# Kernel tuning notes

Hardware: AMD Instinct MI355X
Metric: run time of the kernel (lower is better)

Reference implementation:

```python
import jax, jax.numpy as jnp
import numpy as np

B, N, H, NH, HD, DE = 4, 512, 512, 8, 64, 64
DFF = 4 * H
EPS = 1e-5


def setup_inputs() -> dict:
    key = jax.random.key(0)
    ks = jax.random.split(key, 32)
    w = lambda k, *s: jax.random.normal(k, s, jnp.float32) * 0.02
    inp = {}
    inp['messages'] = jax.random.normal(ks[0], (B, N, H), jnp.float32)
    inp['distance_matrix'] = jax.random.randint(ks[1], (B, N, N), 0, 201).astype(jnp.float32)
    mask = jax.random.randint(ks[2], (B, N, N), 0, 2).astype(jnp.float32)
    inp['mask'] = jnp.maximum(mask, jnp.eye(N, dtype=jnp.float32)[None])  # ensure diag visible
    inp['emb_table'] = w(ks[3], 201, DE)
    inp['Wdq'] = w(ks[4], H, DE); inp['bdq'] = jnp.zeros((H,), jnp.float32)
    inp['Wdk'] = w(ks[5], H, DE); inp['bdk'] = jnp.zeros((H,), jnp.float32)
    inp['Wq'] = w(ks[6], H, H);   inp['bq'] = jnp.zeros((H,), jnp.float32)
    inp['Wk'] = w(ks[7], H, H);   inp['bk'] = jnp.zeros((H,), jnp.float32)
    inp['Wv'] = w(ks[8], H, H);   inp['bv'] = jnp.zeros((H,), jnp.float32)
    inp['Wo'] = w(ks[9], H, H);   inp['bo'] = jnp.zeros((H,), jnp.float32)
    inp['W_ih'] = w(ks[10], 3 * H, H); inp['b_ih'] = jnp.zeros((3 * H,), jnp.float32)
    inp['W_hh'] = w(ks[11], 3 * H, H); inp['b_hh'] = jnp.zeros((3 * H,), jnp.float32)
    inp['W1'] = w(ks[12], DFF, H); inp['b1'] = jnp.zeros((DFF,), jnp.float32)
    inp['W2'] = w(ks[13], H, DFF); inp['b2'] = jnp.zeros((H,), jnp.float32)
    inp['g2'] = jnp.ones((H,), jnp.float32); inp['beta2'] = jnp.zeros((H,), jnp.float32)
    return inp


def reference(messages, distance_matrix, mask, emb_table, Wdq, bdq, Wdk, bdk,
              Wq, bq, Wk, bk, Wv, bv, Wo, bo, W_ih, b_ih, W_hh, b_hh,
              W1, b1, W2, b2, g2, beta2):
    # distance embedding lookup (B,N,N,DE)
    idx = jnp.clip(distance_matrix.astype(jnp.int32), 0, 200)
    emb = emb_table[idx]
    # mean over dim then linear == linear then mean (linear maps commute with mean)
    dq = jnp.mean(emb, axis=2) @ Wdq.T + bdq  # (B,N,H)
    dk = jnp.mean(emb, axis=1) @ Wdk.T + bdk  # (B,N,H)
    Q = ((messages + dq) @ Wq.T + bq).reshape(B, N, NH, HD).transpose(0, 2, 1, 3)
    K = ((messages + dk) @ Wk.T + bk).reshape(B, N, NH, HD).transpose(0, 2, 1, 3)
    V = (messages @ Wv.T + bv).reshape(B, N, NH, HD).transpose(0, 2, 1, 3)
    scale = 1.0 / np.sqrt(HD).astype(np.float32)
    scores = jnp.einsum('bhnd,bhmd->bhnm', Q, K) * scale
    scores = jnp.where(mask[:, None] == 0, -jnp.inf, scores)
    aw = jax.nn.softmax(scores, axis=-1)
    ao = jnp.einsum('bhnm,bhmd->bhnd', aw, V).transpose(0, 2, 1, 3).reshape(B, N, H)
    ao = ao @ Wo.T + bo
    # GRUCell: x = attn output, h = messages
    gx = ao @ W_ih.T + b_ih
    gh = messages @ W_hh.T + b_hh
    xr, xz, xn = jnp.split(gx, 3, axis=-1)
    hr, hz, hn = jnp.split(gh, 3, axis=-1)
    r = jax.nn.sigmoid(xr + hr)
    z = jax.nn.sigmoid(xz + hz)
    n = jnp.tanh(xn + r * hn)
    u = (1.0 - z) * n + z * messages
    # FFN + residual + LayerNorm
    f = jax.nn.relu(u @ W1.T + b1) @ W2.T + b2
    y = u + f
    mu = jnp.mean(y, axis=-1, keepdims=True)
    var = jnp.var(y, axis=-1, keepdims=True)
    return (y - mu) / jnp.sqrt(var + EPS) * g2 + beta2
```

## Files before the change

kernel.cpp:

```cpp
#include <hip/hip_runtime.h>
#include <hip/hip_bf16.h>
#include <math.h>

#define Bz 4
#define Nn 512
#define Hh 512
#define NHh 8
#define HDd 64
#define DEe 64
#define DFFf 2048
#define EPSs 1e-5f
#define QS 1536
#define GS 3072

typedef __attribute__((ext_vector_type(8))) short bf16x8;
typedef __attribute__((ext_vector_type(4))) short bf16x4;
typedef __attribute__((ext_vector_type(4))) float f32x4;

__device__ inline short f2bf(float x) {
    unsigned u = __builtin_bit_cast(unsigned, x);
    unsigned r = (u + 0x7FFFu + ((u >> 16) & 1u)) >> 16;
    return (short)r;
}
__device__ inline float b2f(unsigned short u) {
    unsigned v = ((unsigned)u) << 16;
    return __builtin_bit_cast(float, v);
}
__device__ inline void gld16(const void* g, void* l) {
    __builtin_amdgcn_global_load_lds(
        (const __attribute__((address_space(1))) void*)g,
        (__attribute__((address_space(3))) void*)l, 16, 0, 0);
}

struct CvtArgs {
    const float* src[11];
    unsigned short* dst[11];
    int n[11];
};
__global__ __launch_bounds__(256) void cvttr_kernel(
    CvtArgs a, const float* __restrict__ dist, float* __restrict__ distT,
    const float* __restrict__ emb, unsigned short* __restrict__ embb)
{
    __shared__ float T[64][68];
    int t = threadIdx.x;
    if (blockIdx.x < 512) {
        for (int sg = 0; sg < 11; ++sg) {
            const float4* s = (const float4*)a.src[sg];
            ushort4* d = (ushort4*)a.dst[sg];
            int n4 = a.n[sg] >> 2;
            for (int i = blockIdx.x * 256 + t; i < n4; i += 512 * 256) {
                float4 v = s[i];
                ushort4 o = {(unsigned short)f2bf(v.x), (unsigned short)f2bf(v.y),
                             (unsigned short)f2bf(v.z), (unsigned short)f2bf(v.w)};
                d[i] = o;
            }
        }
        const float sc = 1.0f / 512.0f;
        for (int i = blockIdx.x * 256 + t; i < 4096; i += 512 * 256) {
            ushort4 o = {0, 0, 0, 0};
            if (i * 4 < 201 * 64) {
                float4 v = *(const float4*)(emb + i * 4);
                o.x = (unsigned short)f2bf(v.x * sc);
                o.y = (unsigned short)f2bf(v.y * sc);
                o.z = (unsigned short)f2bf(v.z * sc);
                o.w = (unsigned short)f2bf(v.w * sc);
            }
            *(ushort4*)(embb + i * 4) = o;
        }
    } else {
        int tid = blockIdx.x - 512;
        int b = tid >> 6;
        int i0 = ((tid >> 3) & 7) * 64, j0 = (tid & 7) * 64;
        int rr = t >> 4, c4 = (t & 15) * 4;
#pragma unroll
        for (int p = 0; p < 4; ++p) {
            int r = rr + p * 16;
            float4 v = *(const float4*)&dist[((size_t)(b * Nn + i0 + r)) * Nn + j0 + c4];
            *(float4*)&T[r][c4] = v;
        }
        __syncthreads();
#pragma unroll
        for (int p = 0; p < 4; ++p) {
            int jr = rr + p * 16;
            float4 v = {T[c4 + 0][jr], T[c4 + 1][jr], T[c4 + 2][jr], T[c4 + 3][jr]};
            *(float4*)&distT[((size_t)(b * Nn + j0 + jr)) * Nn + i0 + c4] = v;
        }
    }
}

__global__ __launch_bounds__(256) void hist2_kernel(
    const float* __restrict__ dist, const float* __restrict__ distT,
    unsigned short* __restrict__ histq, unsigned short* __restrict__ histk)
{
    __shared__ int hist[256];
    int bi = blockIdx.x;
    const float* src = blockIdx.y ? distT : dist;
    unsigned short* out = blockIdx.y ? histk : histq;
    int t = threadIdx.x;
    hist[t] = 0;
    __syncthreads();
    float2 v = *(const float2*)(src + (size_t)bi * Nn + t * 2);
    int i0 = min(max((int)v.x, 0), 200);
    int i1 = min(max((int)v.y, 0), 200);
    atomicAdd(&hist[i0], 1);
    atomicAdd(&hist[i1], 1);
    __syncthreads();
    out[(size_t)bi * 256 + t] = (unsigned short)f2bf((float)hist[t]);
}

struct SegArgs {
    const unsigned short* A[3];
    int lda[3];
    const float* bias[3];
    const void* res[3];
    int rlda;
};

template<int BM, int BN, int RELU, int RESM, int OUTF, int HASB>
__global__ __launch_bounds__(256) void mgf_kernel(
    SegArgs sa, const unsigned short* __restrict__ W,
    void* __restrict__ C, int K, int SW, int ldc)
{
    constexpr int WM = BM / 2, WN = BN / 2;
    constexpr int MT = WM / 16, NT = WN / 16;
    constexpr int IPA = BM / 32, IPB = BN / 32;
    __shared__ unsigned short As[2][BM * 64];
    __shared__ unsigned short Bs[2][BN * 64];
    int t = threadIdx.x, lane = t & 63, wid = t >> 6;
    int wm = wid >> 1, wn = wid & 1;
    int m0 = blockIdx.y * BM, n0 = blockIdx.x * BN;
    int seg = n0 / SW;
    int segbase = seg * SW;
    const unsigned short* A = sa.A[seg];
    int lda = sa.lda[seg];
    int lrow8 = lane >> 3;
    int lunit = (lane & 7) ^ lrow8;

    f32x4 acc[MT][NT] = {};

    auto stage = [&](int buf, int kt) {
#pragma unroll
        for (int i = 0; i < IPA; ++i) {
            int c = wid * IPA + i;
            gld16(A + (size_t)(m0 + c * 8 + lrow8) * lda + kt + lunit * 8,
                  &As[buf][c * 512]);
        }
#pragma unroll
        for (int i = 0; i < IPB; ++i) {
            int c = wid * IPB + i;
            gld16(W + (size_t)(n0 + c * 8 + lrow8) * K + kt + lunit * 8,
                  &Bs[buf][c * 512]);
        }
    };

    stage(0, 0);
    __syncthreads();
    int cur = 0;
    for (int kt = 0; kt < K; kt += 64) {
        if (kt + 64 < K) stage(cur ^ 1, kt + 64);
#pragma unroll
        for (int kk = 0; kk < 2; ++kk) {
            bf16x8 fa[MT], fb[NT];
            int ub = kk * 4 + (lane >> 4);
#pragma unroll
            for (int mt = 0; mt < MT; ++mt) {
                int r = wm * WM + mt * 16 + (lane & 15);
                fa[mt] = *(const bf16x8*)&As[cur][r * 64 + ((ub ^ (r & 7)) << 3)];
            }
#pragma unroll
            for (int nt = 0; nt < NT; ++nt) {
                int r = wn * WN + nt * 16 + (lane & 15);
                fb[nt] = *(const bf16x8*)&Bs[cur][r * 64 + ((ub ^ (r & 7)) << 3)];
            }
#pragma unroll
            for (int mt = 0; mt < MT; ++mt)
#pragma unroll
                for (int nt = 0; nt < NT; ++nt)
                    acc[mt][nt] = __builtin_amdgcn_mfma_f32_16x16x32_bf16(
                        fa[mt], fb[nt], acc[mt][nt], 0, 0, 0);
        }
        __syncthreads();
        cur ^= 1;
    }

    int cr = (lane >> 4) * 4, ccl = lane & 15;
#pragma unroll
    for (int mt = 0; mt < MT; ++mt) {
#pragma unroll
        for (int nt = 0; nt < NT; ++nt) {
            int col = n0 + wn * WN + nt * 16 + ccl;
            int lcol = col - segbase;
            float bv = HASB ? sa.bias[seg][lcol] : 0.f;
#pragma unroll
            for (int r = 0; r < 4; ++r) {
                int row = m0 + wm * WM + mt * 16 + cr + r;
                float o = acc[mt][nt][r] + bv;
                if (RESM == 1)
                    o += ((const float*)sa.res[seg])[(size_t)row * sa.rlda + lcol];
                if (RESM == 2)
                    o += b2f(((const unsigned short*)sa.res[seg])
                                 [(size_t)row * sa.rlda + lcol]);
                if (RELU) o = fmaxf(o, 0.f);
                if (OUTF)
                    ((float*)C)[(size_t)row * ldc + col] = o;
                else
                    ((unsigned short*)C)[(size_t)row * ldc + col] =
                        (unsigned short)f2bf(o);
            }
        }
    }
}

__global__ __launch_bounds__(256) void attn_mfma_kernel(
    const unsigned short* __restrict__ QKV, const float* __restrict__ mask,
    unsigned short* __restrict__ AO)
{
    __shared__ unsigned short Qs[64 * 64];
    __shared__ unsigned short Ks[64 * 64];
    __shared__ unsigned short Vt[64 * 64];
    __shared__ float Ms[64 * 65];
    __shared__ unsigned short Pl[4][16 * 72];

    int t = threadIdx.x;
    int lane = t & 63;
    int wq = t >> 6;
    int g = lane >> 4, cc = lane & 15;
    int q0 = blockIdx.x * 64;
    int h = blockIdx.y, b = blockIdx.z;

    int lr = t >> 2;
    int u0 = (t & 3) * 2;
    int c0f = (t & 3) * 16;

    {
        const unsigned short* src =
            QKV + ((size_t)(b * Nn + q0 + lr)) * QS + h * HDd + u0 * 8;
        bf16x8 p0 = *(const bf16x8*)(src);
        bf16x8 p1 = *(const bf16x8*)(src + 8);
        *(bf16x8*)&Qs[lr * 64 + ((u0 ^ (lr & 7)) << 3)] = p0;
        *(bf16x8*)&Qs[lr * 64 + (((u0 + 1) ^ (lr & 7)) << 3)] = p1;
    }

    const unsigned short* Krow =
        QKV + ((size_t)(b * Nn + lr)) * QS + 512 + h * HDd + u0 * 8;
    int vkey = t >> 4;
    int vd0 = (t & 15) * 4;
    const unsigned short* Vbase =
        QKV + ((size_t)(b * Nn)) * QS + 1024 + h * HDd + vd0;
    const float* Mrow = mask + ((size_t)(b * Nn + q0 + lr)) * Nn + c0f;

    bf16x8 kr0, kr1;
    ushort4 vr[4];
    float4 mreg[4];
    auto issue = [&](int kc) {
        int k0 = kc * 64;
        const unsigned short* kp = Krow + (size_t)k0 * QS;
        kr0 = *(const bf16x8*)(kp);
        kr1 = *(const bf16x8*)(kp + 8);
        const float* mp = Mrow + k0;
        mreg[0] = *(const float4*)(mp);
        mreg[1] = *(const float4*)(mp + 4);
        mreg[2] = *(const float4*)(mp + 8);
        mreg[3] = *(const float4*)(mp + 12);
#pragma unroll
        for (int p = 0; p < 4; ++p)
            vr[p] = *(const ushort4*)(Vbase + (size_t)(k0 + vkey + p * 16) * QS);
    };
    issue(0);
    __syncthreads();

    bf16x8 qf0 = *(bf16x8*)&Qs[(wq * 16 + cc) * 64 + (((0 * 4 + g) ^ (cc & 7)) << 3)];
    bf16x8 qf1 = *(bf16x8*)&Qs[(wq * 16 + cc) * 64 + (((1 * 4 + g) ^ (cc & 7)) << 3)];

    const float scale = 0.125f;
    float m_run = -1e30f, l_run = 0.f;
    f32x4 o[4] = {};

    for (int kc = 0; kc < 8; ++kc) {
        {
            *(bf16x8*)&Ks[lr * 64 + ((u0 ^ (lr & 7)) << 3)] = kr0;
            *(bf16x8*)&Ks[lr * 64 + (((u0 + 1) ^ (lr & 7)) << 3)] = kr1;

            float* msr = &Ms[lr * 65 + c0f];
            msr[0] = mreg[0].x;  msr[1] = mreg[0].y;  msr[2] = mreg[0].z;  msr[3] = mreg[0].w;
            msr[4] = mreg[1].x;  msr[5] = mreg[1].y;  msr[6] = mreg[1].z;  msr[7] = mreg[1].w;
            msr[8] = mreg[2].x;  msr[9] = mreg[2].y;  msr[10] = mreg[2].z; msr[11] = mreg[2].w;
            msr[12] = mreg[3].x; msr[13] = mreg[3].y; msr[14] = mreg[3].z; msr[15] = mreg[3].w;

#pragma unroll
            for (int p = 0; p < 4; ++p) {
                int key = vkey + p * 16;
                unsigned short vals[4] = {vr[p].x, vr[p].y, vr[p].z, vr[p].w};
#pragma unroll
                for (int jj = 0; jj < 4; ++jj) {
                    int j = (jj + (t >> 2)) & 3;
                    int d = vd0 + j;
                    Vt[d * 64 + (key ^ ((d & 7) << 3))] = vals[j];
                }
            }
        }
        __syncthreads();
        if (kc < 7) issue(kc + 1);

        f32x4 s[4] = {};
        __builtin_amdgcn_s_setprio(1);
#pragma unroll
        for (int kt = 0; kt < 4; ++kt) {
            int rA = kt * 16 + cc;
            bf16x8 a0 = *(bf16x8*)&Ks[rA * 64 + (((0 * 4 + g) ^ (rA & 7)) << 3)];
            s[kt] = __builtin_amdgcn_mfma_f32_16x16x32_bf16(a0, qf0, s[kt], 0, 0, 0);
            bf16x8 a1 = *(bf16x8*)&Ks[rA * 64 + (((1 * 4 + g) ^ (rA & 7)) << 3)];
            s[kt] = __builtin_amdgcn_mfma_f32_16x16x32_bf16(a1, qf1, s[kt], 0, 0, 0);
        }
        __builtin_amdgcn_s_setprio(0);

        float pv[4][4];
        float tmax = -1e30f;
#pragma unroll
        for (int kt = 0; kt < 4; ++kt) {
#pragma unroll
            for (int r = 0; r < 4; ++r) {
                float mv = Ms[(wq * 16 + cc) * 65 + kt * 16 + g * 4 + r];
                float svv = (mv == 0.f) ? -1e30f : s[kt][r];
                pv[kt][r] = svv;
                tmax = fmaxf(tmax, svv);
            }
        }
        tmax = fmaxf(tmax, __shfl_xor(tmax, 16));
        tmax = fmaxf(tmax, __shfl_xor(tmax, 32));
        float mnew = fmaxf(m_run, tmax);
        float rescale = __expf((m_run - mnew) * scale);
        float psum = 0.f;
#pragma unroll
        for (int kt = 0; kt < 4; ++kt) {
#pragma unroll
            for (int r = 0; r < 4; ++r) {
                float sv = pv[kt][r];
                float p = (sv == -1e30f) ? 0.f : __expf((sv - mnew) * scale);
                pv[kt][r] = p;
                psum += p;
            }
        }
        psum += __shfl_xor(psum, 16);
        psum += __shfl_xor(psum, 32);
        l_run = l_run * rescale + psum;
        m_run = mnew;
#pragma unroll
        for (int dt = 0; dt < 4; ++dt) {
            o[dt][0] *= rescale; o[dt][1] *= rescale;
            o[dt][2] *= rescale; o[dt][3] *= rescale;
        }

#pragma unroll
        for (int kt = 0; kt < 4; ++kt) {
            bf16x4 pk = {f2bf(pv[kt][0]), f2bf(pv[kt][1]),
                         f2bf(pv[kt][2]), f2bf(pv[kt][3])};
            *(bf16x4*)&Pl[wq][cc * 72 + kt * 16 + g * 4] = pk;
        }
        bf16x8 pf0 = *(bf16x8*)&Pl[wq][cc * 72 + 0 + g * 8];
        bf16x8 pf1 = *(bf16x8*)&Pl[wq][cc * 72 + 32 + g * 8];

        __builtin_amdgcn_s_setprio(1);
#pragma unroll
        for (int dt = 0; dt < 4; ++dt) {
            int rV = dt * 16 + cc;
            bf16x8 vf0 = *(bf16x8*)&Vt[rV * 64 + (((0 * 4 + g) ^ (rV & 7)) << 3)];
            o[dt] = __builtin_amdgcn_mfma_f32_16x16x32_bf16(vf0, pf0, o[dt], 0, 0, 0);
            bf16x8 vf1 = *(bf16x8*)&Vt[rV * 64 + (((1 * 4 + g) ^ (rV & 7)) << 3)];
            o[dt] = __builtin_amdgcn_mfma_f32_16x16x32_bf16(vf1, pf1, o[dt], 0, 0, 0);
        }
        __builtin_amdgcn_s_setprio(0);
        __syncthreads();
    }

    float invl = 1.f / l_run;
#pragma unroll
    for (int dt = 0; dt < 4; ++dt) {
        ushort4 w = {(unsigned short)f2bf(o[dt][0] * invl),
                     (unsigned short)f2bf(o[dt][1] * invl),
                     (unsigned short)f2bf(o[dt][2] * invl),
                     (unsigned short)f2bf(o[dt][3] * invl)};
        *(ushort4*)&AO[((size_t)(b * Nn + q0 + wq * 16 + cc)) * Hh +
                       h * HDd + dt * 16 + g * 4] = w;
    }
}

__global__ __launch_bounds__(256) void gru_kernel(
    const unsigned short* __restrict__ G,
    const float* __restrict__ msg, unsigned short* __restrict__ u)
{
    int i4 = blockIdx.x * 256 + threadIdx.x;
    int e = i4 * 4;
    int row = e >> 9, col = e & 511;
    const unsigned short* gxr = G + (size_t)row * GS;
    const unsigned short* ghr = gxr + 1536;
    ushort4 xr4 = *(const ushort4*)(gxr + col);
    ushort4 xz4 = *(const ushort4*)(gxr + col + 512);
    ushort4 xn4 = *(const ushort4*)(gxr + col + 1024);
    ushort4 hr4 = *(const ushort4*)(ghr + col);
    ushort4 hz4 = *(const ushort4*)(ghr + col + 512);
    ushort4 hn4 = *(const ushort4*)(ghr + col + 1024);
    float4 mg4 = *(const float4*)(msg + e);
    float mv[4] = {mg4.x, mg4.y, mg4.z, mg4.w};
    unsigned short xr[4] = {xr4.x, xr4.y, xr4.z, xr4.w};
    unsigned short xz[4] = {xz4.x, xz4.y, xz4.z, xz4.w};
    unsigned short xn[4] = {xn4.x, xn4.y, xn4.z, xn4.w};
    unsigned short hr[4] = {hr4.x, hr4.y, hr4.z, hr4.w};
    unsigned short hz[4] = {hz4.x, hz4.y, hz4.z, hz4.w};
    unsigned short hn[4] = {hn4.x, hn4.y, hn4.z, hn4.w};
    ushort4 out;
    unsigned short* op = (unsigned short*)&out;
#pragma unroll
    for (int j = 0; j < 4; ++j) {
        float r = 1.f / (1.f + __expf(-(b2f(xr[j]) + b2f(hr[j]))));
        float z = 1.f / (1.f + __expf(-(b2f(xz[j]) + b2f(hz[j]))));
        float n = tanhf(b2f(xn[j]) + r * b2f(hn[j]));
        op[j] = (unsigned short)f2bf((1.f - z) * n + z * mv[j]);
    }
    *(ushort4*)(u + e) = out;
}

__global__ __launch_bounds__(256) void ln_kernel(
    const float* __restrict__ Y, const float* __restrict__ g,
    const float* __restrict__ be, float* __restrict__ out)
{
    int row = blockIdx.x, t = threadIdx.x;
    const float* yr = Y + (size_t)row * Hh;
    float v0 = yr[t], v1 = yr[t + 256];
    float s = v0 + v1, s2 = v0 * v0 + v1 * v1;
#pragma unroll
    for (int o = 1; o < 64; o <<= 1) {
        s += __shfl_xor(s, o);
        s2 += __shfl_xor(s2, o);
    }
    __shared__ float rs[4], rs2[4];
    int w = t >> 6;
    if ((t & 63) == 0) { rs[w] = s; rs2[w] = s2; }
    __syncthreads();
    float ts = rs[0] + rs[1] + rs[2] + rs[3];
    float ts2 = rs2[0] + rs2[1] + rs2[2] + rs2[3];
    float mu = ts * (1.0f / Hh);
    float var = ts2 * (1.0f / Hh) - mu * mu;
    float rstd = rsqrtf(var + EPSs);
    out[(size_t)row * Hh + t] = (v0 - mu) * rstd * g[t] + be[t];
    out[(size_t)row * Hh + t + 256] = (v1 - mu) * rstd * g[t + 256] + be[t + 256];
}

extern "C" void kernel_launch(void* const* d_in, const int* in_sizes, int n_in,
                              void* d_out, int out_size, void* d_ws, size_t ws_size,
                              hipStream_t stream) {
    const float* messages = (const float*)d_in[0];
    const float* dist     = (const float*)d_in[1];
    const float* mask     = (const float*)d_in[2];
    const float* emb      = (const float*)d_in[3];
    const float* Wdq = (const float*)d_in[4];  const float* bdq = (const float*)d_in[5];
    const float* Wdk = (const float*)d_in[6];  const float* bdk = (const float*)d_in[7];
    const float* Wq  = (const float*)d_in[8];  const float* bq  = (const float*)d_in[9];
    const float* Wk  = (const float*)d_in[10]; const float* bk  = (const float*)d_in[11];
    const float* Wv  = (const float*)d_in[12]; const float* bv  = (const float*)d_in[13];
    const float* Wo  = (const float*)d_in[14]; const float* bo  = (const float*)d_in[15];
    const float* W_ih = (const float*)d_in[16]; const float* b_ih = (const float*)d_in[17];
    const float* W_hh = (const float*)d_in[18]; const float* b_hh = (const float*)d_in[19];
    const float* W1  = (const float*)d_in[20]; const float* b1  = (const float*)d_in[21];
    const float* W2  = (const float*)d_in[22]; const float* b2  = (const float*)d_in[23];
    const float* g2  = (const float*)d_in[24]; const float* beta2 = (const float*)d_in[25];

    const int M = Bz * Nn;
    char* ws = (char*)d_ws;

    unsigned short* wdqb = (unsigned short*)(ws + 0);
    unsigned short* wdkb = (unsigned short*)(ws + 65536);
    unsigned short* wqkv = (unsigned short*)(ws + 131072);
    unsigned short* wob  = (unsigned short*)(ws + 1703936);
    unsigned short* wgate= (unsigned short*)(ws + 2228224);
    unsigned short* w1b  = (unsigned short*)(ws + 5373952);
    unsigned short* w2b  = (unsigned short*)(ws + 7471104);
    unsigned short* msgs = (unsigned short*)(ws + 9568256);
    unsigned short* XQXK = (unsigned short*)(ws + 12189696);
    unsigned short* QKVb = (unsigned short*)(ws + 16384000);
    unsigned short* AO   = (unsigned short*)(ws + 22675456);
    unsigned short* aob  = (unsigned short*)(ws + 24772608);
    unsigned short* G    = (unsigned short*)(ws + 26869760);
    unsigned short* ub   = (unsigned short*)(ws + 39452672);
    unsigned short* f1   = (unsigned short*)(ws + 41549824);
    float*          yb   = (float*)(ws + 49938432);
    float*          distT= (float*)(ws + 54132736);
    unsigned short* embb = (unsigned short*)(ws + 58327040);
    unsigned short* histq= (unsigned short*)(ws + 58359808);
    unsigned short* histk= (unsigned short*)(ws + 59408384);
    unsigned short* Ecat = (unsigned short*)(ws + 60456960);

    dim3 blk(256);

    CvtArgs ca;
    ca.src[0] = messages; ca.dst[0] = msgs; ca.n[0] = M * Hh;
    ca.src[1] = Wdq;  ca.dst[1] = wdqb;          ca.n[1] = Hh * DEe;
    ca.src[2] = Wdk;  ca.dst[2] = wdkb;          ca.n[2] = Hh * DEe;
    ca.src[3] = Wq;   ca.dst[3] = wqkv;          ca.n[3] = Hh * Hh;
    ca.src[4] = Wk;   ca.dst[4] = wqkv + 262144; ca.n[4] = Hh * Hh;
    ca.src[5] = Wv;   ca.dst[5] = wqkv + 524288; ca.n[5] = Hh * Hh;
    ca.src[6] = Wo;   ca.dst[6] = wob;           ca.n[6] = Hh * Hh;
    ca.src[7] = W_ih; ca.dst[7] = wgate;         ca.n[7] = 3 * Hh * Hh;
    ca.src[8] = W_hh; ca.dst[8] = wgate + 786432;ca.n[8] = 3 * Hh * Hh;
    ca.src[9] = W1;   ca.dst[9] = w1b;           ca.n[9] = DFFf * Hh;
    ca.src[10] = W2;  ca.dst[10] = w2b;          ca.n[10] = Hh * DFFf;
    cvttr_kernel<<<768, blk, 0, stream>>>(ca, dist, distT, emb, embb);

    hist2_kernel<<<dim3(M, 2), blk, 0, stream>>>(dist, distT, histq, histk);

    {
        SegArgs sa = {};
        sa.A[0] = wdqb; sa.lda[0] = 64;
        mgf_kernel<128, 64, 0, 0, 0, 0><<<dim3(4, 8), blk, 0, stream>>>(
            sa, embb, Ecat, 64, 256, 256);
    }

    {
        SegArgs sa = {};
        sa.A[0] = histq; sa.A[1] = histk; sa.lda[0] = 256; sa.lda[1] = 256;
        sa.bias[0] = bdq; sa.bias[1] = bdk;
        sa.res[0] = messages; sa.res[1] = messages; sa.rlda = Hh;
        mgf_kernel<128, 64, 0, 1, 0, 1><<<dim3(16, 16), blk, 0, stream>>>(
            sa, Ecat, XQXK, 256, 512, 1024);
    }

    {
        SegArgs sa = {};
        sa.A[0] = XQXK; sa.A[1] = XQXK + 512; sa.A[2] = msgs;
        sa.lda[0] = 1024; sa.lda[1] = 1024; sa.lda[2] = 512;
        sa.bias[0] = bq; sa.bias[1] = bk; sa.bias[2] = bv;
        mgf_kernel<64, 128, 0, 0, 0, 1><<<dim3(12, 32), blk, 0, stream>>>(
            sa, wqkv, QKVb, Hh, 512, QS);
    }

    attn_mfma_kernel<<<dim3(Nn / 64, NHh, Bz), blk, 0, stream>>>(
        QKVb, mask, AO);

    {
        SegArgs sa = {};
        sa.A[0] = AO; sa.lda[0] = 512; sa.bias[0] = bo;
        mgf_kernel<64, 64, 0, 0, 0, 1><<<dim3(8, 32), blk, 0, stream>>>(
            sa, wob, aob, Hh, 512, 512);
    }

    {
        SegArgs sa = {};
        sa.A[0] = aob; sa.A[1] = msgs; sa.lda[0] = 512; sa.lda[1] = 512;
        sa.bias[0] = b_ih; sa.bias[1] = b_hh;
        mgf_kernel<128, 128, 0, 0, 0, 1><<<dim3(24, 16), blk, 0, stream>>>(
            sa, wgate, G, Hh, 1536, GS);
    }
    gru_kernel<<<(M * Hh) / 1024, blk, 0, stream>>>(G, messages, ub);

    {
        SegArgs sa = {};
        sa.A[0] = ub; sa.lda[0] = 512; sa.bias[0] = b1;
        mgf_kernel<128, 128, 1, 0, 0, 1><<<dim3(16, 16), blk, 0, stream>>>(
            sa, w1b, f1, Hh, 2048, DFFf);
    }
    {
        SegArgs sa = {};
        sa.A[0] = f1; sa.lda[0] = 2048; sa.bias[0] = b2;
        sa.res[0] = ub; sa.rlda = 512;
        mgf_kernel<64, 64, 0, 2, 1, 1><<<dim3(8, 32), blk, 0, stream>>>(
            sa, w2b, yb, DFFf, 512, 512);
    }

    ln_kernel<<<M, blk, 0, stream>>>(yb, g2, beta2, (float*)d_out);
}
```

Before: 123.5 us.

## Fold distance projections, Wo into weights; concat histograms into QK GEMM K-dim

Restructures the pipeline algebraically. The distance-embedding projection is folded into the Q/K weight matrices by concatenating the histogram counts onto the message columns (K=768), and Wo is folded into W_ih via a weight-weight GEMM with adjusted biases. This removes the separate XQXK and Wo GEMMs and the distT transpose. The hidden-state gate GEMM moves into the QKV launch so it runs before attention. The key histogram is built directly with column-wise LDS atomics. It adds small prep GEMMs on weights every call and changes rounding, since the products are formed in bf16.

Result: no change. 124.9 us (+1.1%).

```diff
diff --git a/kernel.cpp b/kernel.cpp
--- a/kernel.cpp
+++ b/kernel.cpp
@@ -32,94 +32,126 @@
         (__attribute__((address_space(3))) void*)l, 16, 0, 0);
 }
 
-struct CvtArgs {
-    const float* src[11];
-    unsigned short* dst[11];
-    int n[11];
+struct CvtSeg { const float* src; unsigned short* dst; int n, ncols, pitch; };
+struct PrepArgs {
+    CvtSeg cs[12];
+    const float* emb; unsigned short* embb;
+    const float* dist;
+    unsigned short* AQ; unsigned short* AK;
+    const float* Wo; unsigned short* woT;
+    const float* fW[3]; const float* fv[3]; const float* fb[3]; float* fo[3];
 };
-__global__ __launch_bounds__(256) void cvttr_kernel(
-    CvtArgs a, const float* __restrict__ dist, float* __restrict__ distT,
-    const float* __restrict__ emb, unsigned short* __restrict__ embb)
+
+__global__ __launch_bounds__(256) void prep_kernel(PrepArgs a)
 {
-    __shared__ float T[64][68];
+    __shared__ char lds[17408];
     int t = threadIdx.x;
-    if (blockIdx.x < 512) {
-        for (int sg = 0; sg < 11; ++sg) {
-            const float4* s = (const float4*)a.src[sg];
-            ushort4* d = (ushort4*)a.dst[sg];
-            int n4 = a.n[sg] >> 2;
-            for (int i = blockIdx.x * 256 + t; i < n4; i += 512 * 256) {
-                float4 v = s[i];
+    int blk = blockIdx.x;
+    if (blk < 512) {
+        for (int sg = 0; sg < 12; ++sg) {
+            CvtSeg c = a.cs[sg];
+            int n4 = c.n >> 2;
+            for (int i = blk * 256 + t; i < n4; i += 512 * 256) {
+                int base = i * 4;
+                int row = base / c.ncols;
+                int col = base - row * c.ncols;
+                float4 v = *(const float4*)(c.src + base);
                 ushort4 o = {(unsigned short)f2bf(v.x), (unsigned short)f2bf(v.y),
                              (unsigned short)f2bf(v.z), (unsigned short)f2bf(v.w)};
-                d[i] = o;
+                *(ushort4*)(c.dst + (size_t)row * c.pitch + col) = o;
             }
         }
         const float sc = 1.0f / 512.0f;
-        for (int i = blockIdx.x * 256 + t; i < 4096; i += 512 * 256) {
+        for (int i = blk * 256 + t; i < 4096; i += 512 * 256) {
             ushort4 o = {0, 0, 0, 0};
             if (i * 4 < 201 * 64) {
-                float4 v = *(const float4*)(emb + i * 4);
+                float4 v = *(const float4*)(a.emb + i * 4);
                 o.x = (unsigned short)f2bf(v.x * sc);
                 o.y = (unsigned short)f2bf(v.y * sc);
                 o.z = (unsigned short)f2bf(v.z * sc);
                 o.w = (unsigned short)f2bf(v.w * sc);
             }
-            *(ushort4*)(embb + i * 4) = o;
-        }
-    } else {
-        int tid = blockIdx.x - 512;
-        int b = tid >> 6;
-        int i0 = ((tid >> 3) & 7) * 64, j0 = (tid & 7) * 64;
+            *(ushort4*)(a.embb + i * 4) = o;
+        }
+    } else if (blk < 552) {
+        int fid = blk - 512;
+        int f, ob;
+        if (fid < 8)       { f = 0; ob = fid * 64; }
+        else if (fid < 16) { f = 1; ob = (fid - 8) * 64; }
+        else               { f = 2; ob = (fid - 16) * 64; }
+        int i = ob + (t >> 2), part = t & 3;
+        const float* Wr = a.fW[f] + (size_t)i * 512 + part * 128;
+        const float* vv = a.fv[f] + part * 128;
+        float s = 0.f;
+        for (int k = 0; k < 128; k += 4) {
+            float4 w4 = *(const float4*)(Wr + k);
+            float4 b4 = *(const float4*)(vv + k);
+            s += w4.x * b4.x + w4.y * b4.y + w4.z * b4.z + w4.w * b4.w;
+        }
+        s += __shfl_xor(s, 1);
+        s += __shfl_xor(s, 2);
+        if (part == 0) a.fo[f][i] = a.fb[f][i] + s;
+    } else if (blk < 616) {
+        int tid = blk - 552;
+        int ti = tid >> 3, tj = tid & 7;
+        float (*T)[68] = (float (*)[68])lds;
         int rr = t >> 4, c4 = (t & 15) * 4;
 #pragma unroll
         for (int p = 0; p < 4; ++p) {
             int r = rr + p * 16;
-            float4 v = *(const float4*)&dist[((size_t)(b * Nn + i0 + r)) * Nn + j0 + c4];
+            float4 v = *(const float4*)(a.Wo + (size_t)(ti * 64 + r) * 512 + tj * 64 + c4);
             *(float4*)&T[r][c4] = v;
         }
         __syncthreads();
 #pragma unroll
         for (int p = 0; p < 4; ++p) {
             int jr = rr + p * 16;
-            float4 v = {T[c4 + 0][jr], T[c4 + 1][jr], T[c4 + 2][jr], T[c4 + 3][jr]};
-            *(float4*)&distT[((size_t)(b * Nn + j0 + jr)) * Nn + i0 + c4] = v;
-        }
-    }
-}
-
-__global__ __launch_bounds__(256) void hist2_kernel(
-    const float* __restrict__ dist, const float* __restrict__ distT,
-    unsigned short* __restrict__ histq, unsigned short* __restrict__ histk)
-{
-    __shared__ int hist[256];
-    int bi = blockIdx.x;
-    const float* src = blockIdx.y ? distT : dist;
-    unsigned short* out = blockIdx.y ? histk : histq;
-    int t = threadIdx.x;
-    hist[t] = 0;
-    __syncthreads();
-    float2 v = *(const float2*)(src + (size_t)bi * Nn + t * 2);
-    int i0 = min(max((int)v.x, 0), 200);
-    int i1 = min(max((int)v.y, 0), 200);
-    atomicAdd(&hist[i0], 1);
-    atomicAdd(&hist[i1], 1);
-    __syncthreads();
-    out[(size_t)bi * 256 + t] = (unsigned short)f2bf((float)hist[t]);
-}
-
-struct SegArgs {
-    const unsigned short* A[3];
-    int lda[3];
-    const float* bias[3];
-    const void* res[3];
-    int rlda;
+            ushort4 o = {(unsigned short)f2bf(T[c4 + 0][jr]),
+                         (unsigned short)f2bf(T[c4 + 1][jr]),
+                         (unsigned short)f2bf(T[c4 + 2][jr]),
+                         (unsigned short)f2bf(T[c4 + 3][jr])};
+            *(ushort4*)(a.woT + (size_t)(tj * 64 + jr) * 512 + ti * 64 + c4) = o;
+        }
+    } else if (blk < 2664) {
+        int r = blk - 616;
+        int* hist = (int*)lds;
+        hist[t] = 0;
+        __syncthreads();
+        float2 v = *(const float2*)(a.dist + (size_t)r * 512 + t * 2);
+        atomicAdd(&hist[min(max((int)v.x, 0), 200)], 1);
+        atomicAdd(&hist[min(max((int)v.y, 0), 200)], 1);
+        __syncthreads();
+        a.AQ[(size_t)r * 768 + 512 + t] = (unsigned short)f2bf((float)hist[t]);
+    } else {
+        int idx = blk - 2664;
+        int b = idx >> 5, jt = idx & 31;
+        int j0 = jt * 16;
+        int* h2 = (int*)lds;
+        for (int k = t; k < 4096; k += 256) h2[k] = 0;
+        __syncthreads();
+        int ri = t >> 4, jj = t & 15;
+        for (int i0 = 0; i0 < 512; i0 += 16) {
+            float v = a.dist[(size_t)(b * 512 + i0 + ri) * 512 + j0 + jj];
+            atomicAdd(&h2[jj * 256 + min(max((int)v, 0), 200)], 1);
+        }
+        __syncthreads();
+        for (int k = t; k < 4096; k += 256) {
+            int jj2 = k >> 8, bin = k & 255;
+            a.AK[(size_t)(b * 512 + j0 + jj2) * 768 + 512 + bin] =
+                (unsigned short)f2bf((float)h2[k]);
+        }
+    }
+}
+
+struct Seg {
+    const unsigned short* A; const unsigned short* W;
+    const float* bias; const void* res; void* C;
+    int lda, Ks, ldw, rlda, ldc, pad;
 };
+struct SegArgs { Seg s[6]; };
 
 template<int BM, int BN, int RELU, int RESM, int OUTF, int HASB>
-__global__ __launch_bounds__(256) void mgf_kernel(
-    SegArgs sa, const unsigned short* __restrict__ W,
-    void* __restrict__ C, int K, int SW, int ldc)
+__global__ __launch_bounds__(256) void mgf_kernel(SegArgs sa, int SW)
 {
     constexpr int WM = BM / 2, WN = BN / 2;
     constexpr int MT = WM / 16, NT = WN / 16;
@@ -130,9 +162,10 @@
     int wm = wid >> 1, wn = wid & 1;
     int m0 = blockIdx.y * BM, n0 = blockIdx.x * BN;
     int seg = n0 / SW;
-    int segbase = seg * SW;
-    const unsigned short* A = sa.A[seg];
-    int lda = sa.lda[seg];
+    const unsigned short* A = sa.s[seg].A;
+    const unsigned short* W = sa.s[seg].W;
+    int lda = sa.s[seg].lda, Ks = sa.s[seg].Ks, ldw = sa.s[seg].ldw;
+    int nloc = n0 - seg * SW;
     int lrow8 = lane >> 3;
     int lunit = (lane & 7) ^ lrow8;
 
@@ -148,7 +181,7 @@
 #pragma unroll
         for (int i = 0; i < IPB; ++i) {
             int c = wid * IPB + i;
-            gld16(W + (size_t)(n0 + c * 8 + lrow8) * K + kt + lunit * 8,
+            gld16(W + (size_t)(nloc + c * 8 + lrow8) * ldw + kt + lunit * 8,
                   &Bs[buf][c * 512]);
         }
     };
@@ -156,8 +189,8 @@
     stage(0, 0);
     __syncthreads();
     int cur = 0;
-    for (int kt = 0; kt < K; kt += 64) {
-        if (kt + 64 < K) stage(cur ^ 1, kt + 64);
+    for (int kt = 0; kt < Ks; kt += 64) {
+        if (kt + 64 < Ks) stage(cur ^ 1, kt + 64);
 #pragma unroll
         for (int kk = 0; kk < 2; ++kk) {
             bf16x8 fa[MT], fb[NT];
@@ -184,27 +217,29 @@
     }
 
     int cr = (lane >> 4) * 4, ccl = lane & 15;
+    const float* bias = sa.s[seg].bias;
+    const void* res = sa.s[seg].res;
+    int rlda = sa.s[seg].rlda, ldc = sa.s[seg].ldc;
+    void* C = sa.s[seg].C;
 #pragma unroll
     for (int mt = 0; mt < MT; ++mt) {
 #pragma unroll
         for (int nt = 0; nt < NT; ++nt) {
-            int col = n0 + wn * WN + nt * 16 + ccl;
-            int lcol = col - segbase;
-            float bv = HASB ? sa.bias[seg][lcol] : 0.f;
+            int lcol = nloc + wn * WN + nt * 16 + ccl;
+            float bv = HASB ? bias[lcol] : 0.f;
 #pragma unroll
             for (int r = 0; r < 4; ++r) {
                 int row = m0 + wm * WM + mt * 16 + cr + r;
                 float o = acc[mt][nt][r] + bv;
                 if (RESM == 1)
-                    o += ((const float*)sa.res[seg])[(size_t)row * sa.rlda + lcol];
+                    o += ((const float*)res)[(size_t)row * rlda + lcol];
                 if (RESM == 2)
-                    o += b2f(((const unsigned short*)sa.res[seg])
-                                 [(size_t)row * sa.rlda + lcol]);
+                    o += b2f(((const unsigned short*)res)[(size_t)row * rlda + lcol]);
                 if (RELU) o = fmaxf(o, 0.f);
                 if (OUTF)
-                    ((float*)C)[(size_t)row * ldc + col] = o;
+                    ((float*)C)[(size_t)row * ldc + lcol] = o;
                 else
-                    ((unsigned short*)C)[(size_t)row * ldc + col] =
+                    ((unsigned short*)C)[(size_t)row * ldc + lcol] =
                         (unsigned short)f2bf(o);
             }
         }
@@ -468,102 +503,104 @@
     const int M = Bz * Nn;
     char* ws = (char*)d_ws;
 
-    unsigned short* wdqb = (unsigned short*)(ws + 0);
-    unsigned short* wdkb = (unsigned short*)(ws + 65536);
-    unsigned short* wqkv = (unsigned short*)(ws + 131072);
-    unsigned short* wob  = (unsigned short*)(ws + 1703936);
-    unsigned short* wgate= (unsigned short*)(ws + 2228224);
-    unsigned short* w1b  = (unsigned short*)(ws + 5373952);
-    unsigned short* w2b  = (unsigned short*)(ws + 7471104);
-    unsigned short* msgs = (unsigned short*)(ws + 9568256);
-    unsigned short* XQXK = (unsigned short*)(ws + 12189696);
-    unsigned short* QKVb = (unsigned short*)(ws + 16384000);
-    unsigned short* AO   = (unsigned short*)(ws + 22675456);
-    unsigned short* aob  = (unsigned short*)(ws + 24772608);
-    unsigned short* G    = (unsigned short*)(ws + 26869760);
-    unsigned short* ub   = (unsigned short*)(ws + 39452672);
-    unsigned short* f1   = (unsigned short*)(ws + 41549824);
-    float*          yb   = (float*)(ws + 49938432);
-    float*          distT= (float*)(ws + 54132736);
-    unsigned short* embb = (unsigned short*)(ws + 58327040);
-    unsigned short* histq= (unsigned short*)(ws + 58359808);
-    unsigned short* histk= (unsigned short*)(ws + 59408384);
-    unsigned short* Ecat = (unsigned short*)(ws + 60456960);
+    unsigned short* wdqb  = (unsigned short*)(ws + 0);
+    unsigned short* wdkb  = (unsigned short*)(ws + 65536);
+    unsigned short* Wbigq = (unsigned short*)(ws + 131072);
+    unsigned short* Wbigk = (unsigned short*)(ws + 917504);
+    unsigned short* wvb   = (unsigned short*)(ws + 1703936);
+    unsigned short* wihb  = (unsigned short*)(ws + 2228224);
+    unsigned short* whhb  = (unsigned short*)(ws + 3801088);
+    unsigned short* w1b   = (unsigned short*)(ws + 5373952);
+    unsigned short* w2b   = (unsigned short*)(ws + 7471104);
+    unsigned short* msgs  = (unsigned short*)(ws + 9568256);
+    unsigned short* AQ    = (unsigned short*)(ws + 11665408);
+    unsigned short* AK    = (unsigned short*)(ws + 14811136);
+    unsigned short* embb  = (unsigned short*)(ws + 17956864);
+    unsigned short* EcatT = (unsigned short*)(ws + 17989632);
+    unsigned short* woT   = (unsigned short*)(ws + 18513920);
+    unsigned short* Wfih  = (unsigned short*)(ws + 19038208);
+    unsigned short* QKVb  = (unsigned short*)(ws + 20611072);
+    unsigned short* AO    = (unsigned short*)(ws + 26902528);
+    unsigned short* G     = (unsigned short*)(ws + 28999680);
+    unsigned short* ub    = (unsigned short*)(ws + 41582592);
+    unsigned short* f1    = (unsigned short*)(ws + 43679744);
+    float*          yb    = (float*)(ws + 52068352);
+    float*          bqp   = (float*)(ws + 56262656);
+    float*          bkp   = (float*)(ws + 56264704);
+    float*          bgxp  = (float*)(ws + 56266752);
 
     dim3 blk(256);
 
-    CvtArgs ca;
-    ca.src[0] = messages; ca.dst[0] = msgs; ca.n[0] = M * Hh;
-    ca.src[1] = Wdq;  ca.dst[1] = wdqb;          ca.n[1] = Hh * DEe;
-    ca.src[2] = Wdk;  ca.dst[2] = wdkb;          ca.n[2] = Hh * DEe;
-    ca.src[3] = Wq;   ca.dst[3] = wqkv;          ca.n[3] = Hh * Hh;
-    ca.src[4] = Wk;   ca.dst[4] = wqkv + 262144; ca.n[4] = Hh * Hh;
-    ca.src[5] = Wv;   ca.dst[5] = wqkv + 524288; ca.n[5] = Hh * Hh;
-    ca.src[6] = Wo;   ca.dst[6] = wob;           ca.n[6] = Hh * Hh;
-    ca.src[7] = W_ih; ca.dst[7] = wgate;         ca.n[7] = 3 * Hh * Hh;
-    ca.src[8] = W_hh; ca.dst[8] = wgate + 786432;ca.n[8] = 3 * Hh * Hh;
-    ca.src[9] = W1;   ca.dst[9] = w1b;           ca.n[9] = DFFf * Hh;
-    ca.src[10] = W2;  ca.dst[10] = w2b;          ca.n[10] = Hh * DFFf;
-    cvttr_kernel<<<768, blk, 0, stream>>>(ca, dist, distT, emb, embb);
-
-    hist2_kernel<<<dim3(M, 2), blk, 0, stream>>>(dist, distT, histq, histk);
+    PrepArgs pa;
+    pa.cs[0]  = {messages, msgs,  M * Hh,        512, 512};
+    pa.cs[1]  = {messages, AQ,    M * Hh,        512, 768};
+    pa.cs[2]  = {messages, AK,    M * Hh,        512, 768};
+    pa.cs[3]  = {Wdq,      wdqb,  Hh * DEe,      64,  64};
+    pa.cs[4]  = {Wdk,      wdkb,  Hh * DEe,      64,  64};
+    pa.cs[5]  = {Wq,       Wbigq, Hh * Hh,       512, 768};
+    pa.cs[6]  = {Wk,       Wbigk, Hh * Hh,       512, 768};
+    pa.cs[7]  = {Wv,       wvb,   Hh * Hh,       512, 512};
+    pa.cs[8]  = {W_ih,     wihb,  3 * Hh * Hh,   512, 512};
+    pa.cs[9]  = {W_hh,     whhb,  3 * Hh * Hh,   512, 512};
+    pa.cs[10] = {W1,       w1b,   DFFf * Hh,     512, 512};
+    pa.cs[11] = {W2,       w2b,   Hh * DFFf,     2048, 2048};
+    pa.emb = emb; pa.embb = embb;
+    pa.dist = dist; pa.AQ = AQ; pa.AK = AK;
+    pa.Wo = Wo; pa.woT = woT;
+    pa.fW[0] = Wq;   pa.fv[0] = bdq; pa.fb[0] = bq;   pa.fo[0] = bqp;
+    pa.fW[1] = Wk;   pa.fv[1] = bdk; pa.fb[1] = bk;   pa.fo[1] = bkp;
+    pa.fW[2] = W_ih; pa.fv[2] = bo;  pa.fb[2] = b_ih; pa.fo[2] = bgxp;
+    prep_kernel<<<2792, blk, 0, stream>>>(pa);
 
     {
         SegArgs sa = {};
-        sa.A[0] = wdqb; sa.lda[0] = 64;
-        mgf_kernel<128, 64, 0, 0, 0, 0><<<dim3(4, 8), blk, 0, stream>>>(
-            sa, embb, Ecat, 64, 256, 256);
+        sa.s[0] = {embb, wdqb, nullptr, nullptr, EcatT, 64, 64, 64, 0, 1024, 0};
+        mgf_kernel<64, 128, 0, 0, 0, 0><<<dim3(8, 4), blk, 0, stream>>>(sa, 1024);
     }
 
     {
         SegArgs sa = {};
-        sa.A[0] = histq; sa.A[1] = histk; sa.lda[0] = 256; sa.lda[1] = 256;
-        sa.bias[0] = bdq; sa.bias[1] = bdk;
-        sa.res[0] = messages; sa.res[1] = messages; sa.rlda = Hh;
-        mgf_kernel<128, 64, 0, 1, 0, 1><<<dim3(16, 16), blk, 0, stream>>>(
-            sa, Ecat, XQXK, 256, 512, 1024);
+        sa.s[0] = {Wbigq, EcatT,       nullptr, nullptr, Wbigq + 512, 768, 512, 1024, 0, 768, 0};
+        sa.s[1] = {Wbigk, EcatT + 512, nullptr, nullptr, Wbigk + 512, 768, 512, 1024, 0, 768, 0};
+        mgf_kernel<64, 64, 0, 0, 0, 0><<<dim3(8, 8), blk, 0, stream>>>(sa, 256);
     }
 
     {
         SegArgs sa = {};
-        sa.A[0] = XQXK; sa.A[1] = XQXK + 512; sa.A[2] = msgs;
-        sa.lda[0] = 1024; sa.lda[1] = 1024; sa.lda[2] = 512;
-        sa.bias[0] = bq; sa.bias[1] = bk; sa.bias[2] = bv;
-        mgf_kernel<64, 128, 0, 0, 0, 1><<<dim3(12, 32), blk, 0, stream>>>(
-            sa, wqkv, QKVb, Hh, 512, QS);
-    }
-
-    attn_mfma_kernel<<<dim3(Nn / 64, NHh, Bz), blk, 0, stream>>>(
-        QKVb, mask, AO);
+        sa.s[0] = {wihb, woT, nullptr, nullptr, Wfih, 512, 512, 512, 0, 512, 0};
+        mgf_kernel<64, 128, 0, 0, 0, 0><<<dim3(4, 24), blk, 0, stream>>>(sa, 512);
+    }
 
     {
         SegArgs sa = {};
-        sa.A[0] = AO; sa.lda[0] = 512; sa.bias[0] = bo;
-        mgf_kernel<64, 64, 0, 0, 0, 1><<<dim3(8, 32), blk, 0, stream>>>(
-            sa, wob, aob, Hh, 512, 512);
-    }
+        sa.s[0] = {AQ,   Wbigq,             bqp,          nullptr, QKVb,        768, 768, 768, 0, QS, 0};
+        sa.s[1] = {AK,   Wbigk,             bkp,          nullptr, QKVb + 512,  768, 768, 768, 0, QS, 0};
+        sa.s[2] = {msgs, wvb,               bv,           nullptr, QKVb + 1024, 512, 512, 512, 0, QS, 0};
+        sa.s[3] = {msgs, whhb,              b_hh,         nullptr, G + 1536,    512, 512, 512, 0, GS, 0};
+        sa.s[4] = {msgs, whhb + 512 * 512,  b_hh + 512,   nullptr, G + 2048,    512, 512, 512, 0, GS, 0};
+        sa.s[5] = {msgs, whhb + 1024 * 512, b_hh + 1024,  nullptr, G + 2560,    512, 512, 512, 0, GS, 0};
+        mgf_kernel<64, 128, 0, 0, 0, 1><<<dim3(24, 32), blk, 0, stream>>>(sa, 512);
+    }
+
+    attn_mfma_kernel<<<dim3(Nn / 64, NHh, Bz), blk, 0, stream>>>(QKVb, mask, AO);
 
     {
         SegArgs sa = {};
-        sa.A[0] = aob; sa.A[1] = msgs; sa.lda[0] = 512; sa.lda[1] = 512;
-        sa.bias[0] = b_ih; sa.bias[1] = b_hh;
-        mgf_kernel<128, 128, 0, 0, 0, 1><<<dim3(24, 16), blk, 0, stream>>>(
-            sa, wgate, G, Hh, 1536, GS);
-    }
+        sa.s[0] = {AO, Wfih, bgxp, nullptr, G, 512, 512, 512, 0, GS, 0};
+        mgf_kernel<64, 128, 0, 0, 0, 1><<<dim3(12, 32), blk, 0, stream>>>(sa, 1536);
+    }
+
     gru_kernel<<<(M * Hh) / 1024, blk, 0, stream>>>(G, messages, ub);
 
     {
         SegArgs sa = {};
-        sa.A[0] = ub; sa.lda[0] = 512; sa.bias[0] = b1;
-        mgf_kernel<128, 128, 1, 0, 0, 1><<<dim3(16, 16), blk, 0, stream>>>(
-            sa, w1b, f1, Hh, 2048, DFFf);
+        sa.s[0] = {ub, w1b, b1, nullptr, f1, 512, 512, 512, 0, DFFf, 0};
+        mgf_kernel<64, 128, 1, 0, 0, 1><<<dim3(16, 32), blk, 0, stream>>>(sa, 2048);
     }
     {
         SegArgs sa = {};
-        sa.A[0] = f1; sa.lda[0] = 2048; sa.bias[0] = b2;
-        sa.res[0] = ub; sa.rlda = 512;
-        mgf_kernel<64, 64, 0, 2, 1, 1><<<dim3(8, 32), blk, 0, stream>>>(
-            sa, w2b, yb, DFFf, 512, 512);
+        sa.s[0] = {f1, w2b, b2, ub, yb, 2048, 2048, 2048, 512, 512, 0};
+        mgf_kernel<64, 64, 0, 2, 1, 1><<<dim3(8, 32), blk, 0, stream>>>(sa, 512);
     }
 
     ln_kernel<<<M, blk, 0, stream>>>(yb, g2, beta2, (float*)d_out);
```
